# Optimization experiments

Hardware: AMD Instinct MI355X
Metric: run time of the kernel (lower is better)

## Reference

```python
import jax, jax.numpy as jnp
import numpy as np

H = 16; DH = 64; D = H * DH
MEM = 1000            # config.memory_size
KT = 8 + 2            # k_similar + k_contiguous
THRESH = 0.5          # surprise_threshold


def _episodic_scan(k_flat):
    """k_flat: [B,S,D] per-token flattened keys. Sequentially (matching the torch
    per-sample python loop) segment each sequence by surprise, write segment-mean
    events into a FIFO memory, and retrieve top-KT events by cosine similarity
    against the last key. Ragged segments handled via masking (jit-safe)."""
    B, S, _ = k_flat.shape
    mem0 = jnp.zeros((MEM, D), k_flat.dtype)
    mv0 = jnp.zeros((MEM,), bool)

    def body(carry, kf):  # kf: [S,D]
        mem, mv = carry
        # surprise_t = ||k_t - k_{t-1}||, surprise_0 = 0
        diffs = jnp.linalg.norm(kf[1:] - kf[:-1], axis=-1)
        surprise = jnp.concatenate([jnp.zeros((1,), kf.dtype), diffs])
        thr = surprise.mean() + THRESH * jnp.std(surprise, ddof=1)  # torch.std is unbiased
        b = (surprise > thr).at[-1].set(True)  # boundary mask; last index forced
        bi = b.astype(jnp.int32)
        seg = jnp.cumsum(bi) - bi              # exclusive cumsum -> segment id per token
        sums = jax.ops.segment_sum(kf, seg, num_segments=S)
        cnts = jax.ops.segment_sum(jnp.ones((S,), kf.dtype), seg, num_segments=S)
        means = sums / jnp.maximum(cnts, 1.0)[:, None]  # [S,D] segment means (masked ragged)
        newv = jnp.arange(S) < bi.sum()
        # compact valid new events to the front (stable sort preserves order)
        o = jnp.argsort(jnp.logical_not(newv).astype(jnp.int32))
        comb = jnp.concatenate([mem, means[o]], axis=0)        # [MEM+S, D]
        cv = jnp.concatenate([mv, newv[o]], axis=0)
        # FIFO truncation: keep the last MEM valid events
        rank = jnp.cumsum(cv.astype(jnp.int32))
        keep = cv & (rank > rank[-1] - MEM)
        o2 = jnp.argsort(jnp.logical_not(keep).astype(jnp.int32))[:MEM]
        mem, mv = comb[o2], keep[o2]
        # retrieval: cosine similarity of last token's key vs memory, top-KT
        qf = kf[-1]
        qn = jnp.maximum(jnp.linalg.norm(qf), 1e-8)
        mn = jnp.maximum(jnp.linalg.norm(mem, axis=1), 1e-8)
        sims = jnp.where(mv, (mem @ qf) / (mn * qn), -jnp.inf)
        _, idx = jax.lax.top_k(sims, KT)
        return (mem, mv), mem[idx]  # retrieved events [KT, D]

    _, rets = jax.lax.scan(body, (mem0, mv0), k_flat)
    return rets  # [B, KT, D]


def setup_inputs() -> dict:
    key = jax.random.key(0)
    ks = jax.random.split(key, 6)
    B, S = 2, 2048
    return {
        "inputs": jax.random.normal(ks[0], (B, S, D), jnp.float32),
        "attention_mask": jnp.ones((B, S), jnp.int32),
        "Wq": jax.random.normal(ks[1], (D, D), jnp.float32) * 0.02,
        "Wk": jax.random.normal(ks[2], (D, D), jnp.float32) * 0.02,
        "Wv": jax.random.normal(ks[3], (D, D), jnp.float32) * 0.02,
        "Wo": jax.random.normal(ks[4], (D, D), jnp.float32) * 0.02,
    }


def reference(inputs, attention_mask, Wq, Wk, Wv, Wo):
    B, S, _ = inputs.shape
    qf = inputs @ Wq.T  # [B,S,D], per-token layout == keys.transpose(0,1).reshape(S,-1)
    kf = inputs @ Wk.T
    vf = inputs @ Wv.T
    q = qf.reshape(B, S, H, DH).transpose(0, 2, 1, 3)  # [B,H,S,DH]
    k = kf.reshape(B, S, H, DH).transpose(0, 2, 1, 3)
    v = vf.reshape(B, S, H, DH).transpose(0, 2, 1, 3)

    ret = _episodic_scan(kf)                               # [B,KT,D]
    ret_k = ret.reshape(B, KT, H, DH).transpose(0, 2, 1, 3)  # [B,H,KT,DH]
    aug_k = jnp.concatenate([ret_k, k], axis=2)            # [B,H,KT+S,DH]
    aug_v = jnp.concatenate([ret_k, v], axis=2)            # retrieved_v == retrieved_k

    scores = jnp.einsum("bhqd,bhkd->bhqk", q, aug_k) / jnp.sqrt(jnp.float32(DH))
    # ALiBi biases: zero for memory tokens, slopes*(pos_i-pos_j) for real tokens
    pos = jnp.arange(S, dtype=jnp.float32)
    pd = pos[:, None] - pos[None, :]                       # [S,S]
    slopes = 2.0 ** (-8.0 * jnp.arange(1, H + 1, dtype=jnp.float32) / H)
    bias_orig = slopes[None, :, None, None] * pd[None, None]  # [1,H,S,S]
    bias = jnp.concatenate(
        [jnp.zeros((1, H, S, KT), scores.dtype),
         jnp.broadcast_to(bias_orig, (1, H, S, S))], axis=3)
    scores = scores - bias
    # causal over real tokens; memory tokens always visible; attention_mask padded with 1s
    causal = jnp.concatenate(
        [jnp.ones((S, KT), bool), jnp.tril(jnp.ones((S, S), bool))], axis=1)
    aug_mask = jnp.concatenate(
        [jnp.ones((B, KT), jnp.int32), attention_mask], axis=1)
    visible = causal[None, None] & (aug_mask[:, None, None, :] > 0)
    scores = jnp.where(visible, scores, -jnp.inf)
    w = jax.nn.softmax(scores, axis=-1)
    out = jnp.einsum("bhqk,bhkd->bhqd", w, aug_v)
    out = out.transpose(0, 2, 1, 3).reshape(B, S, D)
    return out @ Wo.T
```

## Files before the change

### kernel.cpp

```cpp
#include <hip/hip_runtime.h>
#include <math.h>

#define B_ 2
#define S_ 2048
#define H_ 16
#define DH_ 64
#define D_ 1024
#define MEM_ 1000
#define KT_ 10
#define THRESH_ 0.5
#define BS_ (B_ * S_)
#define EVCAP_ (2 * S_)

typedef float f32x4 __attribute__((ext_vector_type(4)));
typedef short bf16x8 __attribute__((ext_vector_type(8)));
typedef short s16x4 __attribute__((ext_vector_type(4)));

__device__ inline unsigned short f2bf(float f) {
    union { float f; unsigned u; } v; v.f = f;
    unsigned u = v.u;
    unsigned r = (u + 0x7FFFu + ((u >> 16) & 1u)) >> 16;
    return (unsigned short)r;
}
__device__ inline float bf2f(unsigned short h) {
    union { unsigned u; float f; } v; v.u = ((unsigned)h) << 16; return v.f;
}

__device__ __forceinline__ void gload16(const short* gp, const short* lp) {
    __builtin_amdgcn_global_load_lds(
        (__attribute__((address_space(1))) void*)(unsigned long long)gp,
        (__attribute__((address_space(3))) void*)(unsigned)(unsigned long long)lp,
        16, 0, 0);
}

__global__ void init_counters(int* scal) { scal[0] = 0; scal[1] = 0; scal[2] = 0; }

__global__ __launch_bounds__(256) void split_x_kernel(const float* __restrict__ src,
                                                      short* __restrict__ h,
                                                      short* __restrict__ m,
                                                      short* __restrict__ l,
                                                      int n4)
{
    int i = blockIdx.x * 256 + threadIdx.x;
    if (i >= n4) return;
    float4 x = ((const float4*)src)[i];
    float xs[4] = {x.x, x.y, x.z, x.w};
    s16x4 hv, mv, lv;
#pragma unroll
    for (int j = 0; j < 4; ++j) {
        unsigned short hb = f2bf(xs[j]);
        float hf = bf2f(hb);
        float r1 = xs[j] - hf;
        unsigned short mb = f2bf(r1);
        hv[j] = (short)hb; mv[j] = (short)mb;
        float mf = bf2f(mb);
        lv[j] = (short)f2bf(r1 - mf);
    }
    ((s16x4*)h)[i] = hv;
    ((s16x4*)m)[i] = mv;
    ((s16x4*)l)[i] = lv;
}

struct SArgs {
    const float* src[4];
    short* h[4];
    short* m[4];
    short* l[4];
};
__global__ __launch_bounds__(256) void split_w_kernel(SArgs sa)
{
    int y = blockIdx.y;
    int i = blockIdx.x * 256 + threadIdx.x;
    float4 x = ((const float4*)sa.src[y])[i];
    float xs[4] = {x.x, x.y, x.z, x.w};
    s16x4 hv, mv, lv;
    bool wl = (sa.l[y] != nullptr);
#pragma unroll
    for (int j = 0; j < 4; ++j) {
        unsigned short hb = f2bf(xs[j]);
        float hf = bf2f(hb);
        float r1 = xs[j] - hf;
        unsigned short mb = f2bf(r1);
        hv[j] = (short)hb; mv[j] = (short)mb;
        if (wl) {
            float mf = bf2f(mb);
            lv[j] = (short)f2bf(r1 - mf);
        }
    }
    ((s16x4*)sa.h[y])[i] = hv;
    ((s16x4*)sa.m[y])[i] = mv;
    if (wl) ((s16x4*)sa.l[y])[i] = lv;
}

struct G8Args {
    const short* A[4][3];
    const short* B[4][3];
    short* outb[4];
    float* outf[4];
    int gsbase[4];
    int nt;
};

__global__ __launch_bounds__(512, 2) void gemm8(G8Args ga)
{
    __shared__ __align__(16) short Abuf[3][2][4096];
    __shared__ __align__(16) short Bbuf[3][2][4096];

    int wg = blockIdx.x;
    int lin = (wg & 7) * 32 + (wg >> 3);
    int jb = lin >> 4;
    int by = lin & 15;
    int g = jb >> 2;
    int bcol = jb & 3;

    int tid = threadIdx.x;
    int w = tid >> 6, l = tid & 63;
    int wm = w >> 2, wn = w & 3;
    int lg = l >> 4, lc = l & 15;

    const short* A0 = ga.A[g][0]; const short* A1 = ga.A[g][1]; const short* A2 = ga.A[g][2];
    const short* B0 = ga.B[g][0]; const short* B1 = ga.B[g][1]; const short* B2 = ga.B[g][2];
    const int gs0 = ga.gsbase[g];
    const int NT = ga.nt;

    const int u = tid;
    const int vswz = (u & 7) ^ ((u >> 3) & 7);
    const int srow = 2 * (u >> 3) + (vswz >> 2);
    const int skcol = (vswz & 3) * 8;
    const size_t abase = (size_t)(by * 256) * D_ + skcol;
    const size_t bbase = (size_t)(bcol * 256) * D_ + skcol;
    const int dst0 = w * 512;

    auto STAGE_A = [&](int ts, int d) {
        int tt = ts >> 5; int k0 = (ts & 31) << 5;
        const short* At = (tt == 0) ? A0 : ((tt == 1) ? A1 : A2);
        const short* Ab = At + abase + k0;
#pragma unroll
        for (int h = 0; h < 2; ++h)
            gload16(Ab + (size_t)(h * 128 + srow) * D_, &Abuf[d][h][dst0]);
    };
    auto STAGE_B = [&](int ts, int d) {
        int tt = ts >> 5; int k0 = (ts & 31) << 5;
        const short* Bt = (tt == 0) ? B0 : ((tt == 1) ? B1 : B2);
        const short* Bb = Bt + bbase + k0;
#pragma unroll
        for (int h = 0; h < 2; ++h)
            gload16(Bb + (size_t)(h * 128 + srow) * D_, &Bbuf[d][h][dst0]);
    };

    f32x4 acc[8][4] = {};
    const int psa = (((((lc & 1) << 2) | lg)) ^ ((lc >> 1) & 7)) * 8;
    const int rbase = (lc >> 1) * 64;

    STAGE_A(gs0, 0); STAGE_B(gs0, 0);
    STAGE_A(gs0 + 1, 1); STAGE_B(gs0 + 1, 1);
    asm volatile("s_waitcnt vmcnt(4)" ::: "memory");
    asm volatile("s_barrier" ::: "memory");
    __builtin_amdgcn_sched_barrier(0);

    int d = 0, ds = 2;
    for (int t = 0; t < NT; ++t) {
        const short* Ab0 = &Abuf[d][wm][rbase + psa];
        const short* Bb0 = &Bbuf[d][wn >> 1][(wn & 1) * 2048 + rbase + psa];
        bf16x8 bv[4], av[4];
#pragma unroll
        for (int nf = 0; nf < 4; ++nf) bv[nf] = *(const bf16x8*)&Bb0[nf * 512];
#pragma unroll
        for (int mf = 0; mf < 4; ++mf) av[mf] = *(const bf16x8*)&Ab0[mf * 512];
        if (t + 2 < NT) STAGE_A(gs0 + t + 2, ds);
        asm volatile("s_barrier" ::: "memory");
        asm volatile("s_waitcnt lgkmcnt(0)" ::: "memory");
        __builtin_amdgcn_sched_barrier(0);
        __builtin_amdgcn_s_setprio(1);
#pragma unroll
        for (int mf = 0; mf < 4; ++mf)
#pragma unroll
            for (int nf = 0; nf < 4; ++nf)
                acc[mf][nf] = __builtin_amdgcn_mfma_f32_16x16x32_bf16(av[mf], bv[nf], acc[mf][nf], 0, 0, 0);
        __builtin_amdgcn_s_setprio(0);
        asm volatile("s_barrier" ::: "memory");
#pragma unroll
        for (int mf = 0; mf < 4; ++mf) av[mf] = *(const bf16x8*)&Ab0[(4 + mf) * 512];
        if (t + 2 < NT) STAGE_B(gs0 + t + 2, ds);
        asm volatile("s_barrier" ::: "memory");
        asm volatile("s_waitcnt lgkmcnt(0)" ::: "memory");
        __builtin_amdgcn_sched_barrier(0);
        __builtin_amdgcn_s_setprio(1);
#pragma unroll
        for (int mf = 0; mf < 4; ++mf)
#pragma unroll
            for (int nf = 0; nf < 4; ++nf)
                acc[4 + mf][nf] = __builtin_amdgcn_mfma_f32_16x16x32_bf16(av[mf], bv[nf], acc[4 + mf][nf], 0, 0, 0);
        __builtin_amdgcn_s_setprio(0);
        if (t + 2 < NT) asm volatile("s_waitcnt vmcnt(4)" ::: "memory");
        else            asm volatile("s_waitcnt vmcnt(0)" ::: "memory");
        asm volatile("s_barrier" ::: "memory");
        __builtin_amdgcn_sched_barrier(0);
        d = (d == 2) ? 0 : d + 1;
        ds = (ds == 2) ? 0 : ds + 1;
    }

    short* ob = ga.outb[g];
    if (ob) {
#pragma unroll
        for (int mf = 0; mf < 8; ++mf)
#pragma unroll
            for (int nf = 0; nf < 4; ++nf)
#pragma unroll
                for (int reg = 0; reg < 4; ++reg) {
                    int row = by * 256 + wm * 128 + mf * 16 + lg * 4 + reg;
                    int col = bcol * 256 + wn * 64 + nf * 16 + lc;
                    ob[(size_t)row * D_ + col] = (short)f2bf(acc[mf][nf][reg]);
                }
    } else {
        float* of = ga.outf[g];
#pragma unroll
        for (int mf = 0; mf < 8; ++mf)
#pragma unroll
            for (int nf = 0; nf < 4; ++nf)
#pragma unroll
                for (int reg = 0; reg < 4; ++reg) {
                    int row = by * 256 + wm * 128 + mf * 16 + lg * 4 + reg;
                    int col = bcol * 256 + wn * 64 + nf * 16 + lc;
                    of[(size_t)row * D_ + col] = acc[mf][nf][reg];
                }
    }
}

__global__ __launch_bounds__(256) void transpose_v(const short* __restrict__ vbf,
                                                   short* __restrict__ vbfT)
{
    __shared__ short st[64][70];
    int s0 = blockIdx.x * 64;
    int h = blockIdx.y;
    int b = blockIdx.z;
    int tid = threadIdx.x;
    int r = tid >> 2, cb = (tid & 3) * 16;
    const short* src = vbf + (size_t)(b * S_ + s0 + r) * D_ + h * DH_ + cb;
    *(bf16x8*)&st[r][cb] = *(const bf16x8*)src;
    *(bf16x8*)&st[r][cb + 8] = *(const bf16x8*)(src + 8);
    __syncthreads();
    int c = tid >> 2, sb = (tid & 3) * 16;
    short tmp[16];
#pragma unroll
    for (int i = 0; i < 16; ++i) tmp[i] = st[sb + i][c];
    short* dst = vbfT + ((size_t)(b * H_ + h) * DH_ + c) * S_ + s0 + sb;
    *(bf16x8*)dst = *(bf16x8*)&tmp[0];
    *(bf16x8*)(dst + 8) = *(bf16x8*)&tmp[8];
}

__global__ __launch_bounds__(256) void addk_kernel(float* __restrict__ kf,
                                                   const float* __restrict__ kp1,
                                                   short* __restrict__ kbf)
{
    size_t i = (size_t)blockIdx.x * 256 + threadIdx.x;
    float4 a = ((const float4*)kf)[i];
    float4 b = ((const float4*)kp1)[i];
    float4 s = {a.x + b.x, a.y + b.y, a.z + b.z, a.w + b.w};
    ((float4*)kf)[i] = s;
    s16x4 o;
    o[0] = (short)f2bf(s.x); o[1] = (short)f2bf(s.y);
    o[2] = (short)f2bf(s.z); o[3] = (short)f2bf(s.w);
    ((s16x4*)kbf)[i] = o;
}

__global__ __launch_bounds__(256) void addo4_kernel(const float* __restrict__ p0,
                                                    const float* __restrict__ p1,
                                                    const float* __restrict__ p2,
                                                    const float* __restrict__ p3,
                                                    float* __restrict__ out)
{
    size_t i = (size_t)blockIdx.x * 256 + threadIdx.x;
    float4 a = ((const float4*)p0)[i];
    float4 b = ((const float4*)p1)[i];
    float4 c = ((const float4*)p2)[i];
    float4 d = ((const float4*)p3)[i];
    float4 s = {((a.x + b.x) + c.x) + d.x, ((a.y + b.y) + c.y) + d.y,
                ((a.z + b.z) + c.z) + d.z, ((a.w + b.w) + c.w) + d.w};
    ((float4*)out)[i] = s;
}

__global__ __launch_bounds__(256) void surprise_kernel(const float* __restrict__ kf,
                                                       double* __restrict__ sur)
{
    int t = blockIdx.x;
    int b = blockIdx.y;
    if (t == 0) { if (threadIdx.x == 0) sur[(size_t)b * S_] = 0.0; return; }
    const float* kfb = kf + (size_t)b * S_ * D_;
    __shared__ double red[256];
    double acc = 0.0;
    for (int d = threadIdx.x; d < D_; d += 256) {
        double df = (double)kfb[(size_t)t * D_ + d] - (double)kfb[(size_t)(t - 1) * D_ + d];
        acc += df * df;
    }
    red[threadIdx.x] = acc;
    __syncthreads();
    for (int s = 128; s > 0; s >>= 1) {
        if (threadIdx.x < s) red[threadIdx.x] += red[threadIdx.x + s];
        __syncthreads();
    }
    if (threadIdx.x == 0) sur[(size_t)b * S_ + t] = sqrt(red[0]);
}

__global__ __launch_bounds__(256) void boundary_kernel(const double* __restrict__ sur,
                                                       int* __restrict__ seg_start,
                                                       int* __restrict__ seg_end,
                                                       int* __restrict__ scal)
{
    __shared__ double lsur[S_];
    __shared__ double red[256];
    __shared__ double sh_mean, sh_thr;
    __shared__ int cnt[256];
    int tid = threadIdx.x;
    for (int t = tid; t < S_; t += 256) lsur[t] = sur[t];
    __syncthreads();
    double a = 0.0;
    for (int t = tid; t < S_; t += 256) a += lsur[t];
    red[tid] = a;
    __syncthreads();
    for (int s = 128; s > 0; s >>= 1) {
        if (tid < s) red[tid] += red[tid + s];
        __syncthreads();
    }
    if (tid == 0) sh_mean = red[0] / (double)S_;
    __syncthreads();
    double mean = sh_mean;
    a = 0.0;
    for (int t = tid; t < S_; t += 256) { double d = lsur[t] - mean; a += d * d; }
    red[tid] = a;
    __syncthreads();
    for (int s = 128; s > 0; s >>= 1) {
        if (tid < s) red[tid] += red[tid + s];
        __syncthreads();
    }
    if (tid == 0) sh_thr = mean + THRESH_ * sqrt(red[0] / (double)(S_ - 1));
    __syncthreads();
    double thr = sh_thr;
    bool flg[8];
    int c = 0;
#pragma unroll
    for (int j = 0; j < 8; ++j) {
        int t = tid * 8 + j;
        flg[j] = (lsur[t] > thr) || (t == S_ - 1);
        c += flg[j] ? 1 : 0;
    }
    cnt[tid] = c;
    __syncthreads();
    for (int off = 1; off < 256; off <<= 1) {
        int v = cnt[tid];
        int add = (tid >= off) ? cnt[tid - off] : 0;
        __syncthreads();
        cnt[tid] = v + add;
        __syncthreads();
    }
    int r = (tid == 0) ? 0 : cnt[tid - 1];
#pragma unroll
    for (int j = 0; j < 8; ++j) {
        if (flg[j]) { seg_end[r] = tid * 8 + j; ++r; }
    }
    __syncthreads();
    int n = cnt[255];
    for (int i = tid; i < n; i += 256)
        seg_start[i] = (i == 0) ? 0 : seg_end[i - 1] + 1;
    if (tid == 0) {
        scal[1] = n;
        scal[2] = scal[0];
        scal[0] += n;
    }
}

__global__ __launch_bounds__(256) void seg_means_kernel(const float* __restrict__ kfb,
                                                        float* __restrict__ events,
                                                        const int* __restrict__ seg_start,
                                                        const int* __restrict__ seg_end,
                                                        const int* __restrict__ scal)
{
    int g = blockIdx.x;
    if (g >= scal[1]) return;
    int s = seg_start[g], e = seg_end[g];
    double inv = 1.0 / (double)(e - s + 1);
    size_t obase = (size_t)(scal[2] + g) * D_;
    for (int d = threadIdx.x; d < D_; d += 256) {
        double acc = 0.0;
        for (int r = s; r <= e; ++r) acc += (double)kfb[(size_t)r * D_ + d];
        events[obase + d] = (float)(acc * inv);
    }
}

__global__ __launch_bounds__(256) void sims_kernel(const float* __restrict__ events,
                                                   const float* __restrict__ q,
                                                   float* __restrict__ sims,
                                                   const int* __restrict__ scal)
{
    int e = blockIdx.x;
    int total = scal[0];
    int w = total < MEM_ ? total : MEM_;
    if (e >= w) { if (threadIdx.x == 0) sims[e] = -INFINITY; return; }
    int wstart = total - w;
    const float* ev = events + (size_t)(wstart + e) * D_;
    __shared__ double r1[256], r2[256], r3[256];
    int tid = threadIdx.x;
    double dot = 0.0, n2 = 0.0, q2 = 0.0;
    for (int d = tid; d < D_; d += 256) {
        double ed = ev[d], qd = q[d];
        dot += ed * qd; n2 += ed * ed; q2 += qd * qd;
    }
    r1[tid] = dot; r2[tid] = n2; r3[tid] = q2;
    __syncthreads();
    for (int s = 128; s > 0; s >>= 1) {
        if (tid < s) { r1[tid] += r1[tid + s]; r2[tid] += r2[tid + s]; r3[tid] += r3[tid + s]; }
        __syncthreads();
    }
    if (tid == 0) {
        double mn = sqrt(r2[0]); if (mn < 1e-8) mn = 1e-8;
        double qn = sqrt(r3[0]); if (qn < 1e-8) qn = 1e-8;
        sims[e] = (float)(r1[0] / (mn * qn));
    }
}

__global__ __launch_bounds__(256) void topk_kernel(const float* __restrict__ events,
                                                   float* __restrict__ sims,
                                                   float* __restrict__ retb,
                                                   const int* __restrict__ scal)
{
    int total = scal[0];
    int w = total < MEM_ ? total : MEM_;
    int wstart = total - w;
    __shared__ float bv[256];
    __shared__ int bidx[256];
    __shared__ int chosen;
    int tid = threadIdx.x;
    for (int r = 0; r < KT_; ++r) {
        float best = -INFINITY;
        int bi = 0x7fffffff;
        for (int e = tid; e < w; e += 256) {
            float v = sims[e];
            if (v > best || (v == best && e < bi)) { best = v; bi = e; }
        }
        bv[tid] = best; bidx[tid] = bi;
        __syncthreads();
        for (int s = 128; s > 0; s >>= 1) {
            if (tid < s) {
                if (bv[tid + s] > bv[tid] || (bv[tid + s] == bv[tid] && bidx[tid + s] < bidx[tid])) {
                    bv[tid] = bv[tid + s]; bidx[tid] = bidx[tid + s];
                }
            }
            __syncthreads();
        }
        if (tid == 0) {
            chosen = (r < w) ? bidx[0] : -1;
            if (chosen >= 0) sims[chosen] = -INFINITY;
        }
        __syncthreads();
        int c = chosen;
        if (c >= 0) {
            const float* ev = events + (size_t)(wstart + c) * D_;
            for (int d = tid; d < D_; d += 256) retb[(size_t)r * D_ + d] = ev[d];
        } else {
            for (int d = tid; d < D_; d += 256) retb[(size_t)r * D_ + d] = 0.0f;
        }
        __syncthreads();
    }
}

#define QTT 128
#define KTT 64
__global__ __launch_bounds__(512, 4) void attn_mfma_kernel(const short* __restrict__ qbf,
                                                           const short* __restrict__ kbf,
                                                           const short* __restrict__ vbfT,
                                                           const float* __restrict__ ret,
                                                           const int* __restrict__ amask,
                                                           short* __restrict__ AOh,
                                                           short* __restrict__ AOm)
{
    __shared__ __align__(16) short k_s[KTT][72];
    __shared__ __align__(16) short vT_s[DH_][72];
    __shared__ __align__(16) short p_s[8][16][72];

    const float LOG2E = 1.4426950408889634f;
    int bid = blockIdx.x;
    int xcd = bid & 7;
    int idx = bid >> 3;
    int qtslot = idx >> 2;
    int hbL = idx & 3;
    int qt = (qtslot < 8) ? (15 - qtslot) : (qtslot - 8);
    int hb = xcd * 4 + hbL;
    int h = hb & 15, b = hb >> 4;
    int q0 = qt * QTT;

    int tid = threadIdx.x;
    int w = tid >> 6, l = tid & 63;
    int lg = l >> 4, lc = l & 15;
    int qb = q0 + w * 16;
    float scale2 = 0.125f * LOG2E;
    float slope2 = exp2f(-0.5f * (float)(h + 1)) * LOG2E;

    bf16x8 qfr[2];
#pragma unroll
    for (int half = 0; half < 2; ++half)
        qfr[half] = *(const bf16x8*)(qbf + ((size_t)(b * S_ + qb + lc)) * D_ + h * DH_ + half * 32 + lg * 8);

    float mrow[4], lrow[4], fac[4];
#pragma unroll
    for (int r = 0; r < 4; ++r) { mrow[r] = -INFINITY; lrow[r] = 0.0f; }
    f32x4 O[4] = {};

    int sr = tid >> 3;
    int sc0 = (tid & 7) * 8;

    const short* kptr = kbf + ((size_t)(b * S_ + sr)) * D_ + h * DH_ + sc0;
    const short* vptr = vbfT + ((size_t)(b * H_ + h) * DH_ + sr) * S_ + sc0;

    int ntiles = 2 * (qt + 1);
    bf16x8 kr = *(const bf16x8*)kptr;
    bf16x8 vr = *(const bf16x8*)vptr;

    for (int tile = 0; tile < ntiles; ++tile) {
        int j0 = tile * KTT;
        __syncthreads();
        *(bf16x8*)&k_s[sr][sc0] = kr;
        *(bf16x8*)&vT_s[sr][sc0] = vr;
        __syncthreads();
        if (tile + 1 < ntiles) {
            kr = *(const bf16x8*)(kptr + (size_t)(tile + 1) * KTT * D_);
            vr = *(const bf16x8*)(vptr + (tile + 1) * KTT);
        }

        float sc[4][4];
        int am[4];
#pragma unroll
        for (int kt = 0; kt < 4; ++kt) am[kt] = amask[b * S_ + j0 + kt * 16 + lc];
        bool fullvis = (j0 + 63 <= qb);
#pragma unroll
        for (int kt = 0; kt < 4; ++kt) {
            f32x4 s = {0.0f, 0.0f, 0.0f, 0.0f};
            bf16x8 k0 = *(const bf16x8*)&k_s[kt * 16 + lc][lg * 8];
            bf16x8 k1 = *(const bf16x8*)&k_s[kt * 16 + lc][32 + lg * 8];
            s = __builtin_amdgcn_mfma_f32_16x16x32_bf16(qfr[0], k0, s, 0, 0, 0);
            s = __builtin_amdgcn_mfma_f32_16x16x32_bf16(qfr[1], k1, s, 0, 0, 0);
            int jg = j0 + kt * 16 + lc;
            if (fullvis) {
#pragma unroll
                for (int reg = 0; reg < 4; ++reg) {
                    int qi = qb + lg * 4 + reg;
                    sc[kt][reg] = (am[kt] > 0) ? (s[reg] * scale2 - slope2 * (float)(qi - jg)) : -INFINITY;
                }
            } else {
#pragma unroll
                for (int reg = 0; reg < 4; ++reg) {
                    int qi = qb + lg * 4 + reg;
                    bool vis = (jg <= qi) && (am[kt] > 0);
                    sc[kt][reg] = vis ? (s[reg] * scale2 - slope2 * (float)(qi - jg)) : -INFINITY;
                }
            }
        }

        float pv_[4][4];
#pragma unroll
        for (int reg = 0; reg < 4; ++reg) {
            float tm = fmaxf(fmaxf(sc[0][reg], sc[1][reg]), fmaxf(sc[2][reg], sc[3][reg]));
#pragma unroll
            for (int msk = 1; msk <= 8; msk <<= 1) tm = fmaxf(tm, __shfl_xor(tm, msk));
            float mnew = fmaxf(mrow[reg], tm);
            fac[reg] = exp2f(mrow[reg] - mnew);
            mrow[reg] = mnew;
            float rs = 0.0f;
#pragma unroll
            for (int kt = 0; kt < 4; ++kt) {
                float p = exp2f(sc[kt][reg] - mnew);
                pv_[kt][reg] = p;
                rs += p;
            }
#pragma unroll
            for (int msk = 1; msk <= 8; msk <<= 1) rs += __shfl_xor(rs, msk);
            lrow[reg] = lrow[reg] * fac[reg] + rs;
        }

        int parity = l & 1;
#pragma unroll
        for (int kt = 0; kt < 4; ++kt) {
#pragma unroll
            for (int rp = 0; rp < 4; rp += 2) {
                float s0 = pv_[kt][rp];
                float s1 = pv_[kt][rp + 1];
                float o0 = __shfl_xor(s0, 1);
                float o1 = __shfl_xor(s1, 1);
                float lo, hi; int reg;
                if (parity == 0) { lo = s0; hi = o0; reg = rp; }
                else             { lo = o1; hi = s1; reg = rp + 1; }
                unsigned pk = (unsigned)f2bf(lo) | ((unsigned)f2bf(hi) << 16);
                *(unsigned*)&p_s[w][lg * 4 + reg][kt * 16 + (lc & ~1)] = pk;
            }
        }
        __syncthreads();

#pragma unroll
        for (int db = 0; db < 4; ++db) {
#pragma unroll
            for (int reg = 0; reg < 4; ++reg) O[db][reg] *= fac[reg];
        }
#pragma unroll
        for (int kh = 0; kh < 2; ++kh) {
            bf16x8 a = *(const bf16x8*)&p_s[w][lc][kh * 32 + lg * 8];
#pragma unroll
            for (int db = 0; db < 4; ++db) {
                bf16x8 vb = *(const bf16x8*)&vT_s[db * 16 + lc][kh * 32 + lg * 8];
                O[db] = __builtin_amdgcn_mfma_f32_16x16x32_bf16(a, vb, O[db], 0, 0, 0);
            }
        }
    }

    {
        __syncthreads();
        short kv[8];
        if (sr < KT_) {
            const float* rp = ret + ((size_t)(b * KT_ + sr)) * D_ + h * DH_ + sc0;
            float4 a0 = *(const float4*)rp;
            float4 a1 = *(const float4*)(rp + 4);
            kv[0] = (short)f2bf(a0.x); kv[1] = (short)f2bf(a0.y);
            kv[2] = (short)f2bf(a0.z); kv[3] = (short)f2bf(a0.w);
            kv[4] = (short)f2bf(a1.x); kv[5] = (short)f2bf(a1.y);
            kv[6] = (short)f2bf(a1.z); kv[7] = (short)f2bf(a1.w);
        } else {
#pragma unroll
            for (int i = 0; i < 8; ++i) kv[i] = 0;
        }
        *(bf16x8*)&k_s[sr][sc0] = *(bf16x8*)&kv[0];
        __syncthreads();
        short tv[8];
#pragma unroll
        for (int i = 0; i < 8; ++i) {
            int key = sc0 + i;
            tv[i] = (key < KT_) ? k_s[key][sr] : (short)0;
        }
        *(bf16x8*)&vT_s[sr][sc0] = *(bf16x8*)&tv[0];

        float scm[4];
        {
            f32x4 s = {0.0f, 0.0f, 0.0f, 0.0f};
            bf16x8 k0 = *(const bf16x8*)&k_s[lc][lg * 8];
            bf16x8 k1 = *(const bf16x8*)&k_s[lc][32 + lg * 8];
            s = __builtin_amdgcn_mfma_f32_16x16x32_bf16(qfr[0], k0, s, 0, 0, 0);
            s = __builtin_amdgcn_mfma_f32_16x16x32_bf16(qfr[1], k1, s, 0, 0, 0);
#pragma unroll
            for (int reg = 0; reg < 4; ++reg)
                scm[reg] = (lc < KT_) ? s[reg] * scale2 : -INFINITY;
        }
        float pm[4];
#pragma unroll
        for (int reg = 0; reg < 4; ++reg) {
            float tm = scm[reg];
#pragma unroll
            for (int msk = 1; msk <= 8; msk <<= 1) tm = fmaxf(tm, __shfl_xor(tm, msk));
            float mnew = fmaxf(mrow[reg], tm);
            fac[reg] = exp2f(mrow[reg] - mnew);
            mrow[reg] = mnew;
            float p = exp2f(scm[reg] - mnew);
            pm[reg] = p;
            float rs = p;
#pragma unroll
            for (int msk = 1; msk <= 8; msk <<= 1) rs += __shfl_xor(rs, msk);
            lrow[reg] = lrow[reg] * fac[reg] + rs;
        }
        int parity = l & 1;
#pragma unroll
        for (int kt = 0; kt < 2; ++kt) {
#pragma unroll
            for (int rp = 0; rp < 4; rp += 2) {
                float s0 = (kt == 1) ? 0.0f : pm[rp];
                float s1 = (kt == 1) ? 0.0f : pm[rp + 1];
                float o0 = __shfl_xor(s0, 1);
                float o1 = __shfl_xor(s1, 1);
                float lo, hi; int reg;
                if (parity == 0) { lo = s0; hi = o0; reg = rp; }
                else             { lo = o1; hi = s1; reg = rp + 1; }
                unsigned pk = (unsigned)f2bf(lo) | ((unsigned)f2bf(hi) << 16);
                *(unsigned*)&p_s[w][lg * 4 + reg][kt * 16 + (lc & ~1)] = pk;
            }
        }
        __syncthreads();
#pragma unroll
        for (int db = 0; db < 4; ++db) {
#pragma unroll
            for (int reg = 0; reg < 4; ++reg) O[db][reg] *= fac[reg];
        }
        {
            bf16x8 a = *(const bf16x8*)&p_s[w][lc][lg * 8];
#pragma unroll
            for (int db = 0; db < 4; ++db) {
                bf16x8 vb = *(const bf16x8*)&vT_s[db * 16 + lc][lg * 8];
                O[db] = __builtin_amdgcn_mfma_f32_16x16x32_bf16(a, vb, O[db], 0, 0, 0);
            }
        }
    }

#pragma unroll
    for (int db = 0; db < 4; ++db) {
#pragma unroll
        for (int reg = 0; reg < 4; ++reg) {
            int qi = qb + lg * 4 + reg;
            size_t idx2 = ((size_t)(b * S_ + qi)) * D_ + h * DH_ + db * 16 + lc;
            float o = O[db][reg] / lrow[reg];
            unsigned short hb2 = f2bf(o);
            float hf = bf2f(hb2);
            unsigned short mb = f2bf(o - hf);
            AOh[idx2] = (short)hb2;
            AOm[idx2] = (short)mb;
        }
    }
}

extern "C" void kernel_launch(void* const* d_in, const int* in_sizes, int n_in,
                              void* d_out, int out_size, void* d_ws, size_t ws_size,
                              hipStream_t stream)
{
    const float* X = (const float*)d_in[0];
    const int* amask = (const int*)d_in[1];
    const float* Wq = (const float*)d_in[2];
    const float* Wk = (const float*)d_in[3];
    const float* Wv = (const float*)d_in[4];
    const float* Wo = (const float*)d_in[5];
    float* out = (float*)d_out;

    char* p = (char*)d_ws;
    auto alloc = [&](size_t bytes) -> char* {
        char* r = p; p += (bytes + 255) & ~(size_t)255; return r;
    };
    double* sur = (double*)alloc((size_t)B_ * S_ * sizeof(double));
    float* kacc = (float*)alloc((size_t)2 * BS_ * D_ * sizeof(float));
    float* events = (float*)alloc((size_t)EVCAP_ * D_ * sizeof(float));
    float* ret = (float*)alloc((size_t)B_ * KT_ * D_ * sizeof(float));
    float* sims = (float*)alloc(MEM_ * sizeof(float));
    int* seg_start = (int*)alloc(S_ * sizeof(int));
    int* seg_end = (int*)alloc(S_ * sizeof(int));
    int* scal = (int*)alloc(64);
    short* qbf = (short*)alloc((size_t)BS_ * D_ * sizeof(short));
    short* vbf = (short*)alloc((size_t)BS_ * D_ * sizeof(short));
    short* vbfT = (short*)alloc((size_t)B_ * H_ * DH_ * S_ * sizeof(short));
    short* Xh = (short*)alloc((size_t)BS_ * D_ * sizeof(short));
    short* Xm = (short*)alloc((size_t)BS_ * D_ * sizeof(short));
    short* Xl = (short*)alloc((size_t)BS_ * D_ * sizeof(short));
    short* Wqh = (short*)alloc((size_t)D_ * D_ * sizeof(short));
    short* Wqm = (short*)alloc((size_t)D_ * D_ * sizeof(short));
    short* Wvh = (short*)alloc((size_t)D_ * D_ * sizeof(short));
    short* Wvm = (short*)alloc((size_t)D_ * D_ * sizeof(short));
    short* Woh = (short*)alloc((size_t)D_ * D_ * sizeof(short));
    short* Wom = (short*)alloc((size_t)D_ * D_ * sizeof(short));
    short* Wkh = (short*)alloc((size_t)D_ * D_ * sizeof(short));
    short* Wkm = (short*)alloc((size_t)D_ * D_ * sizeof(short));
    short* Wkl = (short*)alloc((size_t)D_ * D_ * sizeof(short));
    if ((size_t)(p - (char*)d_ws) > ws_size) return;

    float* kf = kacc;
    float* kp1 = kacc + (size_t)BS_ * D_;
    short* kbf = Xl;

    init_counters<<<1, 1, 0, stream>>>(scal);

    int nx4 = BS_ * D_ / 4;
    int nw4 = D_ * D_ / 4;
    split_x_kernel<<<(nx4 + 255) / 256, 256, 0, stream>>>(X, Xh, Xm, Xl, nx4);
    {
        SArgs sa = {};
        sa.src[0] = Wq; sa.h[0] = Wqh; sa.m[0] = Wqm; sa.l[0] = nullptr;
        sa.src[1] = Wk; sa.h[1] = Wkh; sa.m[1] = Wkm; sa.l[1] = Wkl;
        sa.src[2] = Wv; sa.h[2] = Wvh; sa.m[2] = Wvm; sa.l[2] = nullptr;
        sa.src[3] = Wo; sa.h[3] = Woh; sa.m[3] = Wom; sa.l[3] = nullptr;
        split_w_kernel<<<dim3(nw4 / 256, 4), 256, 0, stream>>>(sa);
    }

    {
        G8Args ga = {};
        ga.A[0][0] = Xm;  ga.A[0][1] = Xh;  ga.A[0][2] = Xh;
        ga.B[0][0] = Wqh; ga.B[0][1] = Wqm; ga.B[0][2] = Wqh;
        ga.outb[0] = qbf;
        ga.A[1][0] = Xm;  ga.A[1][1] = Xh;  ga.A[1][2] = Xh;
        ga.B[1][0] = Wvh; ga.B[1][1] = Wvm; ga.B[1][2] = Wvh;
        ga.outb[1] = vbf;
        ga.A[2][0] = Xh;  ga.A[2][1] = Xm;  ga.A[2][2] = Xm;
        ga.B[2][0] = Wkm; ga.B[2][1] = Wkh; ga.B[2][2] = Wkm;
        ga.outf[2] = kf;
        ga.A[3][0] = Xh;  ga.A[3][1] = Xl;  ga.A[3][2] = Xh;
        ga.B[3][0] = Wkl; ga.B[3][1] = Wkh; ga.B[3][2] = Wkh;
        ga.outf[3] = kp1;
        ga.gsbase[0] = 0; ga.gsbase[1] = 0; ga.gsbase[2] = 0; ga.gsbase[3] = 0;
        ga.nt = 96;
        gemm8<<<256, 512, 0, stream>>>(ga);
    }
    transpose_v<<<dim3(S_ / 64, H_, B_), 256, 0, stream>>>(vbf, vbfT);
    addk_kernel<<<BS_ * D_ / 4 / 256, 256, 0, stream>>>(kf, kp1, kbf);

    surprise_kernel<<<dim3(S_, B_), 256, 0, stream>>>(kf, sur);
    for (int b = 0; b < B_; ++b) {
        const float* kfb = kf + (size_t)b * S_ * D_;
        boundary_kernel<<<1, 256, 0, stream>>>(sur + (size_t)b * S_, seg_start, seg_end, scal);
        seg_means_kernel<<<S_, 256, 0, stream>>>(kfb, events, seg_start, seg_end, scal);
        sims_kernel<<<MEM_, 256, 0, stream>>>(events, kfb + (size_t)(S_ - 1) * D_, sims, scal);
        topk_kernel<<<1, 256, 0, stream>>>(events, sims, ret + (size_t)b * KT_ * D_, scal);
    }

    attn_mfma_kernel<<<512, 512, 0, stream>>>(qbf, kbf, vbfT, ret, amask, Xh, Xm);

    {
        float* p2 = events;
        float* p3 = (float*)qbf;
        G8Args ga = {};
        for (int g = 0; g < 4; ++g) {
            ga.A[g][0] = Xm;  ga.A[g][1] = Xh;  ga.A[g][2] = Xh;
            ga.B[g][0] = Woh; ga.B[g][1] = Wom; ga.B[g][2] = Woh;
            ga.gsbase[g] = g * 24;
        }
        ga.outf[0] = kf; ga.outf[1] = kp1; ga.outf[2] = p2; ga.outf[3] = p3;
        ga.nt = 24;
        gemm8<<<256, 512, 0, stream>>>(ga);
        addo4_kernel<<<BS_ * D_ / 4 / 256, 256, 0, stream>>>(kf, kp1, p2, p3, out);
    }
}
```

Measured before the change: 415.3 us.

## Merge split/fixup kernels and batch episodic pipeline across both sequences

```diff
diff --git a/kernel.cpp b/kernel.cpp
--- a/kernel.cpp
+++ b/kernel.cpp
@@ -33,48 +33,31 @@
         16, 0, 0);
 }
 
-__global__ void init_counters(int* scal) { scal[0] = 0; scal[1] = 0; scal[2] = 0; }
-
-__global__ __launch_bounds__(256) void split_x_kernel(const float* __restrict__ src,
-                                                      short* __restrict__ h,
-                                                      short* __restrict__ m,
-                                                      short* __restrict__ l,
-                                                      int n4)
-{
-    int i = blockIdx.x * 256 + threadIdx.x;
-    if (i >= n4) return;
+struct SpArgs {
+    const float* X;
+    short *Xh, *Xm, *Xl;
+    const float* W[4];
+    short *Wh[4], *Wm[4], *Wl[4];
+    int nx4;
+};
+__global__ __launch_bounds__(256) void split_all_kernel(SpArgs sa)
+{
+    int bid = blockIdx.x;
+    const float* src; short *ph, *pm, *pl; int i;
+    if (bid < 4096) {
+        i = bid * 256 + threadIdx.x;
+        if (i >= sa.nx4) return;
+        src = sa.X; ph = sa.Xh; pm = sa.Xm; pl = sa.Xl;
+    } else {
+        int wb = bid - 4096;
+        int y = wb >> 10;
+        i = (wb & 1023) * 256 + threadIdx.x;
+        src = sa.W[y]; ph = sa.Wh[y]; pm = sa.Wm[y]; pl = sa.Wl[y];
+    }
     float4 x = ((const float4*)src)[i];
     float xs[4] = {x.x, x.y, x.z, x.w};
     s16x4 hv, mv, lv;
-#pragma unroll
-    for (int j = 0; j < 4; ++j) {
-        unsigned short hb = f2bf(xs[j]);
-        float hf = bf2f(hb);
-        float r1 = xs[j] - hf;
-        unsigned short mb = f2bf(r1);
-        hv[j] = (short)hb; mv[j] = (short)mb;
-        float mf = bf2f(mb);
-        lv[j] = (short)f2bf(r1 - mf);
-    }
-    ((s16x4*)h)[i] = hv;
-    ((s16x4*)m)[i] = mv;
-    ((s16x4*)l)[i] = lv;
-}
-
-struct SArgs {
-    const float* src[4];
-    short* h[4];
-    short* m[4];
-    short* l[4];
-};
-__global__ __launch_bounds__(256) void split_w_kernel(SArgs sa)
-{
-    int y = blockIdx.y;
-    int i = blockIdx.x * 256 + threadIdx.x;
-    float4 x = ((const float4*)sa.src[y])[i];
-    float xs[4] = {x.x, x.y, x.z, x.w};
-    s16x4 hv, mv, lv;
-    bool wl = (sa.l[y] != nullptr);
+    bool wl = (pl != nullptr);
 #pragma unroll
     for (int j = 0; j < 4; ++j) {
         unsigned short hb = f2bf(xs[j]);
@@ -87,9 +70,9 @@
             lv[j] = (short)f2bf(r1 - mf);
         }
     }
-    ((s16x4*)sa.h[y])[i] = hv;
-    ((s16x4*)sa.m[y])[i] = mv;
-    if (wl) ((s16x4*)sa.l[y])[i] = lv;
+    ((s16x4*)ph)[i] = hv;
+    ((s16x4*)pm)[i] = mv;
+    if (wl) ((s16x4*)pl)[i] = lv;
 }
 
 struct G8Args {
@@ -227,41 +210,43 @@
     }
 }
 
-__global__ __launch_bounds__(256) void transpose_v(const short* __restrict__ vbf,
-                                                   short* __restrict__ vbfT)
-{
-    __shared__ short st[64][70];
-    int s0 = blockIdx.x * 64;
-    int h = blockIdx.y;
-    int b = blockIdx.z;
+__global__ __launch_bounds__(256) void fixup_kernel(const short* __restrict__ vbf,
+                                                    short* __restrict__ vbfT,
+                                                    float* __restrict__ kf,
+                                                    const float* __restrict__ kp1,
+                                                    short* __restrict__ kbf)
+{
+    int bid = blockIdx.x;
     int tid = threadIdx.x;
-    int r = tid >> 2, cb = (tid & 3) * 16;
-    const short* src = vbf + (size_t)(b * S_ + s0 + r) * D_ + h * DH_ + cb;
-    *(bf16x8*)&st[r][cb] = *(const bf16x8*)src;
-    *(bf16x8*)&st[r][cb + 8] = *(const bf16x8*)(src + 8);
-    __syncthreads();
-    int c = tid >> 2, sb = (tid & 3) * 16;
-    short tmp[16];
-#pragma unroll
-    for (int i = 0; i < 16; ++i) tmp[i] = st[sb + i][c];
-    short* dst = vbfT + ((size_t)(b * H_ + h) * DH_ + c) * S_ + s0 + sb;
-    *(bf16x8*)dst = *(bf16x8*)&tmp[0];
-    *(bf16x8*)(dst + 8) = *(bf16x8*)&tmp[8];
-}
-
-__global__ __launch_bounds__(256) void addk_kernel(float* __restrict__ kf,
-                                                   const float* __restrict__ kp1,
-                                                   short* __restrict__ kbf)
-{
-    size_t i = (size_t)blockIdx.x * 256 + threadIdx.x;
-    float4 a = ((const float4*)kf)[i];
-    float4 b = ((const float4*)kp1)[i];
-    float4 s = {a.x + b.x, a.y + b.y, a.z + b.z, a.w + b.w};
-    ((float4*)kf)[i] = s;
-    s16x4 o;
-    o[0] = (short)f2bf(s.x); o[1] = (short)f2bf(s.y);
-    o[2] = (short)f2bf(s.z); o[3] = (short)f2bf(s.w);
-    ((s16x4*)kbf)[i] = o;
+    if (bid < 1024) {
+        __shared__ short st[64][70];
+        int t = bid;
+        int s0 = (t & 31) * 64;
+        int h = (t >> 5) & 15;
+        int b = t >> 9;
+        int r = tid >> 2, cb = (tid & 3) * 16;
+        const short* src = vbf + (size_t)(b * S_ + s0 + r) * D_ + h * DH_ + cb;
+        *(bf16x8*)&st[r][cb] = *(const bf16x8*)src;
+        *(bf16x8*)&st[r][cb + 8] = *(const bf16x8*)(src + 8);
+        __syncthreads();
+        int c = tid >> 2, sb = (tid & 3) * 16;
+        short tmp[16];
+#pragma unroll
+        for (int i = 0; i < 16; ++i) tmp[i] = st[sb + i][c];
+        short* dst = vbfT + ((size_t)(b * H_ + h) * DH_ + c) * S_ + s0 + sb;
+        *(bf16x8*)dst = *(bf16x8*)&tmp[0];
+        *(bf16x8*)(dst + 8) = *(bf16x8*)&tmp[8];
+    } else {
+        size_t i = (size_t)(bid - 1024) * 256 + tid;
+        float4 a = ((const float4*)kf)[i];
+        float4 b = ((const float4*)kp1)[i];
+        float4 s = {a.x + b.x, a.y + b.y, a.z + b.z, a.w + b.w};
+        ((float4*)kf)[i] = s;
+        s16x4 o;
+        o[0] = (short)f2bf(s.x); o[1] = (short)f2bf(s.y);
+        o[2] = (short)f2bf(s.z); o[3] = (short)f2bf(s.w);
+        ((s16x4*)kbf)[i] = o;
+    }
 }
 
 __global__ __launch_bounds__(256) void addo4_kernel(const float* __restrict__ p0,
@@ -302,84 +287,93 @@
     if (threadIdx.x == 0) sur[(size_t)b * S_ + t] = sqrt(red[0]);
 }
 
-__global__ __launch_bounds__(256) void boundary_kernel(const double* __restrict__ sur,
-                                                       int* __restrict__ seg_start,
-                                                       int* __restrict__ seg_end,
-                                                       int* __restrict__ scal)
+__global__ __launch_bounds__(256) void boundary2_kernel(const double* __restrict__ sur,
+                                                        int* __restrict__ seg_start,
+                                                        int* __restrict__ seg_end,
+                                                        int* __restrict__ scal)
 {
     __shared__ double lsur[S_];
     __shared__ double red[256];
     __shared__ double sh_mean, sh_thr;
     __shared__ int cnt[256];
     int tid = threadIdx.x;
-    for (int t = tid; t < S_; t += 256) lsur[t] = sur[t];
-    __syncthreads();
-    double a = 0.0;
-    for (int t = tid; t < S_; t += 256) a += lsur[t];
-    red[tid] = a;
-    __syncthreads();
-    for (int s = 128; s > 0; s >>= 1) {
-        if (tid < s) red[tid] += red[tid + s];
-        __syncthreads();
-    }
-    if (tid == 0) sh_mean = red[0] / (double)S_;
-    __syncthreads();
-    double mean = sh_mean;
-    a = 0.0;
-    for (int t = tid; t < S_; t += 256) { double d = lsur[t] - mean; a += d * d; }
-    red[tid] = a;
-    __syncthreads();
-    for (int s = 128; s > 0; s >>= 1) {
-        if (tid < s) red[tid] += red[tid + s];
-        __syncthreads();
-    }
-    if (tid == 0) sh_thr = mean + THRESH_ * sqrt(red[0] / (double)(S_ - 1));
-    __syncthreads();
-    double thr = sh_thr;
-    bool flg[8];
-    int c = 0;
-#pragma unroll
-    for (int j = 0; j < 8; ++j) {
-        int t = tid * 8 + j;
-        flg[j] = (lsur[t] > thr) || (t == S_ - 1);
-        c += flg[j] ? 1 : 0;
-    }
-    cnt[tid] = c;
-    __syncthreads();
-    for (int off = 1; off < 256; off <<= 1) {
-        int v = cnt[tid];
-        int add = (tid >= off) ? cnt[tid - off] : 0;
-        __syncthreads();
-        cnt[tid] = v + add;
-        __syncthreads();
-    }
-    int r = (tid == 0) ? 0 : cnt[tid - 1];
-#pragma unroll
-    for (int j = 0; j < 8; ++j) {
-        if (flg[j]) { seg_end[r] = tid * 8 + j; ++r; }
-    }
-    __syncthreads();
-    int n = cnt[255];
-    for (int i = tid; i < n; i += 256)
-        seg_start[i] = (i == 0) ? 0 : seg_end[i - 1] + 1;
-    if (tid == 0) {
-        scal[1] = n;
-        scal[2] = scal[0];
-        scal[0] += n;
-    }
-}
-
-__global__ __launch_bounds__(256) void seg_means_kernel(const float* __restrict__ kfb,
+    int running = 0;
+    for (int b = 0; b < B_; ++b) {
+        __syncthreads();
+        for (int t = tid; t < S_; t += 256) lsur[t] = sur[(size_t)b * S_ + t];
+        __syncthreads();
+        double a = 0.0;
+        for (int t = tid; t < S_; t += 256) a += lsur[t];
+        red[tid] = a;
+        __syncthreads();
+        for (int s = 128; s > 0; s >>= 1) {
+            if (tid < s) red[tid] += red[tid + s];
+            __syncthreads();
+        }
+        if (tid == 0) sh_mean = red[0] / (double)S_;
+        __syncthreads();
+        double mean = sh_mean;
+        a = 0.0;
+        for (int t = tid; t < S_; t += 256) { double d = lsur[t] - mean; a += d * d; }
+        red[tid] = a;
+        __syncthreads();
+        for (int s = 128; s > 0; s >>= 1) {
+            if (tid < s) red[tid] += red[tid + s];
+            __syncthreads();
+        }
+        if (tid == 0) sh_thr = mean + THRESH_ * sqrt(red[0] / (double)(S_ - 1));
+        __syncthreads();
+        double thr = sh_thr;
+        bool flg[8];
+        int c = 0;
+#pragma unroll
+        for (int j = 0; j < 8; ++j) {
+            int t = tid * 8 + j;
+            flg[j] = (lsur[t] > thr) || (t == S_ - 1);
+            c += flg[j] ? 1 : 0;
+        }
+        cnt[tid] = c;
+        __syncthreads();
+        for (int off = 1; off < 256; off <<= 1) {
+            int v = cnt[tid];
+            int add = (tid >= off) ? cnt[tid - off] : 0;
+            __syncthreads();
+            cnt[tid] = v + add;
+            __syncthreads();
+        }
+        int r = (tid == 0) ? 0 : cnt[tid - 1];
+        int* se = seg_end + b * S_;
+        int* ss = seg_start + b * S_;
+#pragma unroll
+        for (int j = 0; j < 8; ++j) {
+            if (flg[j]) { se[r] = tid * 8 + j; ++r; }
+        }
+        __syncthreads();
+        int n = cnt[255];
+        for (int i = tid; i < n; i += 256)
+            ss[i] = (i == 0) ? 0 : se[i - 1] + 1;
+        if (tid == 0) {
+            scal[4 + b] = n;
+            scal[6 + b] = running;
+        }
+        running += n;
+        __syncthreads();
+    }
+}
+
+__global__ __launch_bounds__(256) void seg_means_kernel(const float* __restrict__ kf,
                                                         float* __restrict__ events,
                                                         const int* __restrict__ seg_start,
                                                         const int* __restrict__ seg_end,
                                                         const int* __restrict__ scal)
 {
     int g = blockIdx.x;
-    if (g >= scal[1]) return;
-    int s = seg_start[g], e = seg_end[g];
+    int b = blockIdx.y;
+    if (g >= scal[4 + b]) return;
+    const float* kfb = kf + (size_t)b * S_ * D_;
+    int s = seg_start[b * S_ + g], e = seg_end[b * S_ + g];
     double inv = 1.0 / (double)(e - s + 1);
-    size_t obase = (size_t)(scal[2] + g) * D_;
+    size_t obase = (size_t)(scal[6 + b] + g) * D_;
     for (int d = threadIdx.x; d < D_; d += 256) {
         double acc = 0.0;
         for (int r = s; r <= e; ++r) acc += (double)kfb[(size_t)r * D_ + d];
@@ -388,16 +382,19 @@
 }
 
 __global__ __launch_bounds__(256) void sims_kernel(const float* __restrict__ events,
-                                                   const float* __restrict__ q,
+                                                   const float* __restrict__ kf,
                                                    float* __restrict__ sims,
                                                    const int* __restrict__ scal)
 {
     int e = blockIdx.x;
-    int total = scal[0];
+    int b = blockIdx.y;
+    int total = scal[6 + b] + scal[4 + b];
     int w = total < MEM_ ? total : MEM_;
-    if (e >= w) { if (threadIdx.x == 0) sims[e] = -INFINITY; return; }
+    float* sb = sims + b * MEM_;
+    if (e >= w) { if (threadIdx.x == 0) sb[e] = -INFINITY; return; }
     int wstart = total - w;
     const float* ev = events + (size_t)(wstart + e) * D_;
+    const float* q = kf + ((size_t)(b * S_ + S_ - 1)) * D_;
     __shared__ double r1[256], r2[256], r3[256];
     int tid = threadIdx.x;
     double dot = 0.0, n2 = 0.0, q2 = 0.0;
@@ -414,18 +411,21 @@
     if (tid == 0) {
         double mn = sqrt(r2[0]); if (mn < 1e-8) mn = 1e-8;
         double qn = sqrt(r3[0]); if (qn < 1e-8) qn = 1e-8;
-        sims[e] = (float)(r1[0] / (mn * qn));
+        sb[e] = (float)(r1[0] / (mn * qn));
     }
 }
 
 __global__ __launch_bounds__(256) void topk_kernel(const float* __restrict__ events,
                                                    float* __restrict__ sims,
-                                                   float* __restrict__ retb,
+                                                   float* __restrict__ ret,
                                                    const int* __restrict__ scal)
 {
-    int total = scal[0];
+    int b = blockIdx.x;
+    int total = scal[6 + b] + scal[4 + b];
     int w = total < MEM_ ? total : MEM_;
     int wstart = total - w;
+    float* sb = sims + b * MEM_;
+    float* retb = ret + (size_t)b * KT_ * D_;
     __shared__ float bv[256];
     __shared__ int bidx[256];
     __shared__ int chosen;
@@ -434,7 +434,7 @@
         float best = -INFINITY;
         int bi = 0x7fffffff;
         for (int e = tid; e < w; e += 256) {
-            float v = sims[e];
+            float v = sb[e];
             if (v > best || (v == best && e < bi)) { best = v; bi = e; }
         }
         bv[tid] = best; bidx[tid] = bi;
@@ -449,7 +449,7 @@
         }
         if (tid == 0) {
             chosen = (r < w) ? bidx[0] : -1;
-            if (chosen >= 0) sims[chosen] = -INFINITY;
+            if (chosen >= 0) sb[chosen] = -INFINITY;
         }
         __syncthreads();
         int c = chosen;
@@ -730,9 +730,9 @@
     float* kacc = (float*)alloc((size_t)2 * BS_ * D_ * sizeof(float));
     float* events = (float*)alloc((size_t)EVCAP_ * D_ * sizeof(float));
     float* ret = (float*)alloc((size_t)B_ * KT_ * D_ * sizeof(float));
-    float* sims = (float*)alloc(MEM_ * sizeof(float));
-    int* seg_start = (int*)alloc(S_ * sizeof(int));
-    int* seg_end = (int*)alloc(S_ * sizeof(int));
+    float* sims = (float*)alloc((size_t)B_ * MEM_ * sizeof(float));
+    int* seg_start = (int*)alloc((size_t)B_ * S_ * sizeof(int));
+    int* seg_end = (int*)alloc((size_t)B_ * S_ * sizeof(int));
     int* scal = (int*)alloc(64);
     short* qbf = (short*)alloc((size_t)BS_ * D_ * sizeof(short));
     short* vbf = (short*)alloc((size_t)BS_ * D_ * sizeof(short));
@@ -755,18 +755,15 @@
     float* kp1 = kacc + (size_t)BS_ * D_;
     short* kbf = Xl;
 
-    init_counters<<<1, 1, 0, stream>>>(scal);
-
-    int nx4 = BS_ * D_ / 4;
-    int nw4 = D_ * D_ / 4;
-    split_x_kernel<<<(nx4 + 255) / 256, 256, 0, stream>>>(X, Xh, Xm, Xl, nx4);
     {
-        SArgs sa = {};
-        sa.src[0] = Wq; sa.h[0] = Wqh; sa.m[0] = Wqm; sa.l[0] = nullptr;
-        sa.src[1] = Wk; sa.h[1] = Wkh; sa.m[1] = Wkm; sa.l[1] = Wkl;
-        sa.src[2] = Wv; sa.h[2] = Wvh; sa.m[2] = Wvm; sa.l[2] = nullptr;
-        sa.src[3] = Wo; sa.h[3] = Woh; sa.m[3] = Wom; sa.l[3] = nullptr;
-        split_w_kernel<<<dim3(nw4 / 256, 4), 256, 0, stream>>>(sa);
+        SpArgs sa = {};
+        sa.X = X; sa.Xh = Xh; sa.Xm = Xm; sa.Xl = Xl;
+        sa.W[0] = Wq; sa.Wh[0] = Wqh; sa.Wm[0] = Wqm; sa.Wl[0] = nullptr;
+        sa.W[1] = Wk; sa.Wh[1] = Wkh; sa.Wm[1] = Wkm; sa.Wl[1] = Wkl;
+        sa.W[2] = Wv; sa.Wh[2] = Wvh; sa.Wm[2] = Wvm; sa.Wl[2] = nullptr;
+        sa.W[3] = Wo; sa.Wh[3] = Woh; sa.Wm[3] = Wom; sa.Wl[3] = nullptr;
+        sa.nx4 = BS_ * D_ / 4;
+        split_all_kernel<<<4096 + 4096, 256, 0, stream>>>(sa);
     }
 
     {
@@ -787,17 +784,13 @@
         ga.nt = 96;
         gemm8<<<256, 512, 0, stream>>>(ga);
     }
-    transpose_v<<<dim3(S_ / 64, H_, B_), 256, 0, stream>>>(vbf, vbfT);
-    addk_kernel<<<BS_ * D_ / 4 / 256, 256, 0, stream>>>(kf, kp1, kbf);
+    fixup_kernel<<<1024 + BS_ * D_ / 4 / 256, 256, 0, stream>>>(vbf, vbfT, kf, kp1, kbf);
 
     surprise_kernel<<<dim3(S_, B_), 256, 0, stream>>>(kf, sur);
-    for (int b = 0; b < B_; ++b) {
-        const float* kfb = kf + (size_t)b * S_ * D_;
-        boundary_kernel<<<1, 256, 0, stream>>>(sur + (size_t)b * S_, seg_start, seg_end, scal);
-        seg_means_kernel<<<S_, 256, 0, stream>>>(kfb, events, seg_start, seg_end, scal);
-        sims_kernel<<<MEM_, 256, 0, stream>>>(events, kfb + (size_t)(S_ - 1) * D_, sims, scal);
-        topk_kernel<<<1, 256, 0, stream>>>(events, sims, ret + (size_t)b * KT_ * D_, scal);
-    }
+    boundary2_kernel<<<1, 256, 0, stream>>>(sur, seg_start, seg_end, scal);
+    seg_means_kernel<<<dim3(S_, B_), 256, 0, stream>>>(kf, events, seg_start, seg_end, scal);
+    sims_kernel<<<dim3(MEM_, B_), 256, 0, stream>>>(events, kf, sims, scal);
+    topk_kernel<<<B_, 256, 0, stream>>>(events, sims, ret, scal);
 
     attn_mfma_kernel<<<512, 512, 0, stream>>>(qbf, kbf, vbfT, ret, amask, Xh, Xm);
 
```

New measurement: 355.3 us. -14.4%, faster.
